# Kernel optimization log

Hardware: AMD Instinct MI355X
Metric: run time of the kernel (lower is better)

## Reference

```python
import jax, jax.numpy as jnp
import numpy as np

B, T, E, S, H = 1, 2048, 768, 256, 150
E3, E9 = 3 * E, 9 * E


def _lin(k, fan_in, fan_out):
    return jax.random.normal(k, (fan_in, fan_out), jnp.float32) / np.sqrt(fan_in).astype(np.float32)


def _mlp(x, W1, b1, W2, b2, W3, b3):
    # Score module: Linear -> ReLU -> Linear -> ReLU -> Linear (dropout = identity in eval)
    h = jax.nn.relu(x @ W1 + b1)
    h = jax.nn.relu(h @ W2 + b2)
    return h @ W3 + b3


def setup_inputs() -> dict:
    key = jax.random.key(0)
    ks = jax.random.split(key, 16)
    encoded_docs = jax.random.normal(ks[0], (B, T, E), jnp.float32)
    span_start = jnp.sort(jax.random.randint(ks[1], (B, S), 0, T - 16), axis=-1)
    span_width = jax.random.randint(ks[2], (B, S), 0, 16)
    return {
        'encoded_docs': encoded_docs,
        'span_start': span_start,
        'span_width': span_width,
        # attention Score (input dim E)
        'aW1': _lin(ks[3], E, H), 'ab1': jnp.zeros((H,), jnp.float32),
        'aW2': _lin(ks[4], H, H), 'ab2': jnp.zeros((H,), jnp.float32),
        'aW3': _lin(ks[5], H, 1), 'ab3': jnp.zeros((1,), jnp.float32),
        # mention Score (input dim 3E)
        'mW1': _lin(ks[6], E3, H), 'mb1': jnp.zeros((H,), jnp.float32),
        'mW2': _lin(ks[7], H, H), 'mb2': jnp.zeros((H,), jnp.float32),
        'mW3': _lin(ks[8], H, 1), 'mb3': jnp.zeros((1,), jnp.float32),
        # pairwise Score (input dim 9E)
        'pW1': _lin(ks[9], E9, H), 'pb1': jnp.zeros((H,), jnp.float32),
        'pW2': _lin(ks[10], H, H), 'pb2': jnp.zeros((H,), jnp.float32),
        'pW3': _lin(ks[11], H, 1), 'pb3': jnp.zeros((1,), jnp.float32),
    }


def reference(encoded_docs, span_start, span_width,
              aW1, ab1, aW2, ab2, aW3, ab3,
              mW1, mb1, mW2, mb2, mW3, mb3,
              pW1, pb1, pW2, pb2, pW3, pb3):
    e = encoded_docs  # [B, T, E]
    attn = _mlp(e, aW1, ab1, aW2, ab2, aW3, ab3)  # [B, T, 1]
    # span sums via prefix sums of attn-weighted embeddings (inclusive start..end)
    c = jnp.cumsum(e * attn, axis=1)  # [B, T, E]
    cpad = jnp.concatenate([jnp.zeros_like(c[:, :1]), c], axis=1)  # [B, T+1, E]
    end = jnp.clip(span_start + span_width, 0, T - 1)  # [B, S]
    bidx = jnp.arange(e.shape[0])[:, None]
    e_start = e[bidx, span_start]                      # [B, S, E]
    e_end = e[bidx, end]                               # [B, S, E]
    span_sum = cpad[bidx, end + 1] - cpad[bidx, span_start]  # [B, S, E]
    g = jnp.concatenate([e_start, e_end, span_sum], axis=-1)  # [B, S, 3E]
    m = _mlp(g, mW1, mb1, mW2, mb2, mW3, mb3)  # [B, S, 1]
    # pairwise: concat(g_i, g_j, g_i*g_j) @ pW1 decomposed over the three blocks
    Wa, Wb, Wc = pW1[:E3], pW1[E3:2 * E3], pW1[2 * E3:]
    hi = g @ Wa  # [B, S, H]
    hj = g @ Wb  # [B, S, H]
    hij = jnp.einsum('bie,bje,eh->bijh', g, g, Wc)  # [B, S, S, H]
    h1 = jax.nn.relu(hi[:, :, None, :] + hj[:, None, :, :] + hij + pb1)
    h2 = jax.nn.relu(h1 @ pW2 + pb2)
    s = h2 @ pW3 + pb3  # [B, S, S, 1]
    ext = (m[:, :, None, :] + m[:, None, :, :] + s) / 3.0
    return jnp.clip(ext, 0.0, 1.0)
```

## Files before the change

### kernel.cpp

```cpp
#include <hip/hip_runtime.h>

typedef unsigned short u16;
typedef unsigned int   u32;
typedef short bf16x8 __attribute__((ext_vector_type(8)));
typedef float f32x4  __attribute__((ext_vector_type(4)));

__device__ __forceinline__ u16 f2bf(float f) {
  union { float f; u32 u; } v; v.f = f;
  u32 u = v.u;
  u += 0x7fffu + ((u >> 16) & 1u);
  return (u16)(u >> 16);
}

__device__ __forceinline__ void splitbf(float x, u16& hi, u16& lo) {
  hi = f2bf(x);
  union { u32 u; float f; } r; r.u = (u32)hi << 16;
  lo = f2bf(x - r.f);
}

__device__ __forceinline__ float bflo(u32 p) {
  union { u32 u; float f; } v; v.u = p << 16; return v.f;
}
__device__ __forceinline__ float bfhi(u32 p) {
  union { u32 u; float f; } v; v.u = p & 0xffff0000u; return v.f;
}
__device__ __forceinline__ u32 cvtpk(float lo, float hi) {
  u32 r;
  asm("v_cvt_pk_bf16_f32 %0, %1, %2" : "=v"(r) : "v"(lo), "v"(hi));
  return r;
}
__device__ __forceinline__ void gload_lds16(const void* src, void* dst) {
  __builtin_amdgcn_global_load_lds(
      (const __attribute__((address_space(1))) u32*)src,
      (__attribute__((address_space(3))) u32*)dst, 16, 0, 0);
}

__global__ __launch_bounds__(256) void k_prepT(
    const float* __restrict__ mW1, const float* __restrict__ pW1,
    const float* __restrict__ aW1, const float* __restrict__ aW2,
    const float* __restrict__ mW2, const float* __restrict__ pW2,
    const float* __restrict__ pb1, const float* __restrict__ pb2,
    const float* __restrict__ pW3,
    u16* __restrict__ Wcath, u16* __restrict__ Wcatl,
    u16* __restrict__ aW1Th, u16* __restrict__ aW1Tl,
    u16* __restrict__ Wckg,
    float* __restrict__ aW2p, float* __restrict__ mW2p,
    u16* __restrict__ W2kg, float* __restrict__ pb1p,
    float* __restrict__ pb2p, float* __restrict__ w3p) {
  __shared__ float ls[64][153];
  const int tid = threadIdx.x;
  const int task = blockIdx.y;
  const int e0 = blockIdx.x * 64;
  if (task == 5) {
    const int stride = 36 * 256;
    const int t0 = blockIdx.x * 256 + tid;
    for (int t = t0; t < 152*160; t += stride) {
      int k = t / 160, h = t % 160;
      bool ok = (k < 150 && h < 150);
      aW2p[t] = ok ? aW2[k*150 + h] : 0.f;
      mW2p[t] = ok ? mW2[k*150 + h] : 0.f;
    }
    for (int t = t0; t < 24*1280; t += stride) {
      int kg = t / 1280, rem = t % 1280;
      int s = rem / 160, n = rem % 160;
      int k = kg*8 + s;
      float v = (k < 150 && n < 150) ? pW2[k*150 + n] : 0.f;
      W2kg[(size_t)kg*1280 + n*8 + s] = f2bf(v);
    }
    for (int t = t0; t < 160; t += stride) {
      pb1p[t] = (t < 150) ? pb1[t] : 0.f;
      pb2p[t] = (t < 150) ? pb2[t] : 0.f;
      w3p[t]  = (t < 150) ? pW3[t] : 0.f;
    }
    return;
  }
  if (task == 3 && e0 >= 768) return;
  const float* src;
  if (task == 0)      src = mW1;
  else if (task == 1) src = pW1;
  else if (task == 2) src = pW1 + (size_t)2304 * 150;
  else if (task == 3) src = aW1;
  else                src = pW1 + (size_t)4608 * 150;
  for (int t = tid; t < 9600; t += 256) {
    int r = t / 150, c = t - r * 150;
    ls[r][c] = src[(size_t)(e0 + r) * 150 + c];
  }
  __syncthreads();
  if (task < 3) {
    u16* dh = Wcath + (size_t)task * 160 * 2304;
    u16* dl = Wcatl + (size_t)task * 160 * 2304;
    for (int t = tid; t < 10240; t += 256) {
      int n = t >> 6, r = t & 63;
      float v = (n < 150) ? ls[r][n] : 0.f;
      u16 h, l; splitbf(v, h, l);
      dh[(size_t)n * 2304 + e0 + r] = h;
      dl[(size_t)n * 2304 + e0 + r] = l;
    }
  } else if (task == 3) {
    for (int t = tid; t < 10240; t += 256) {
      int n = t >> 6, r = t & 63;
      float v = (n < 150) ? ls[r][n] : 0.f;
      u16 h, l; splitbf(v, h, l);
      aW1Th[(size_t)n * 768 + e0 + r] = h;
      aW1Tl[(size_t)n * 768 + e0 + r] = l;
    }
  } else {
    for (int t = tid; t < 10240; t += 256) {
      int n = t >> 6, r = t & 63;
      int e = e0 + r;
      float v = (n < 150) ? ls[r][n] : 0.f;
      Wckg[((size_t)(e >> 3) * 160 + n) * 8 + (e & 7)] = f2bf(v);
    }
  }
}

__global__ __launch_bounds__(256) void k_attn1(
    const float* __restrict__ e, const u16* __restrict__ Wh,
    const u16* __restrict__ Wl, float* __restrict__ h1p) {
  __shared__ u16 lXh[32*64], lXl[32*64], lWh[160*64], lWl[160*64];
  const int tid = threadIdx.x, lane = tid & 63, w = tid >> 6;
  const int wm = w & 1, wh = w >> 1;
  const int m0 = blockIdx.x * 32;
  const int z  = blockIdx.y;
  f32x4 acc[5] = {};
  for (int e0 = z*192; e0 < (z+1)*192; e0 += 64) {
    {
      int r = tid >> 3, ec = tid & 7;
      const float* src = e + (size_t)(m0 + r)*768 + e0 + ec*8;
      float4 x0 = *(const float4*)src, x1 = *(const float4*)(src + 4);
      float xs[8] = {x0.x,x0.y,x0.z,x0.w,x1.x,x1.y,x1.z,x1.w};
      u16 hb[8], lb[8];
#pragma unroll
      for (int q = 0; q < 8; ++q) splitbf(xs[q], hb[q], lb[q]);
      int off = (r*128 + ec*16) ^ ((r & 7) << 4);
      *(uint4*)((char*)lXh + off) = make_uint4(
        (u32)hb[0]|((u32)hb[1]<<16), (u32)hb[2]|((u32)hb[3]<<16),
        (u32)hb[4]|((u32)hb[5]<<16), (u32)hb[6]|((u32)hb[7]<<16));
      *(uint4*)((char*)lXl + off) = make_uint4(
        (u32)lb[0]|((u32)lb[1]<<16), (u32)lb[2]|((u32)lb[3]<<16),
        (u32)lb[4]|((u32)lb[5]<<16), (u32)lb[6]|((u32)lb[7]<<16));
    }
#pragma unroll
    for (int t = 0; t < 5; ++t) {
      int c = tid + t*256;
      int h = c >> 3, ec = c & 7;
      int off = (h*128 + ec*16) ^ ((h & 7) << 4);
      *(uint4*)((char*)lWh + off) = *(const uint4*)(Wh + (size_t)h*768 + e0 + ec*8);
      *(uint4*)((char*)lWl + off) = *(const uint4*)(Wl + (size_t)h*768 + e0 + ec*8);
    }
    __syncthreads();
#pragma unroll
    for (int ks = 0; ks < 2; ++ks) {
      int eb = ks*64 + ((lane >> 4) << 4);
      int ar = wm*16 + (lane & 15);
      bf16x8 Ah = *(const bf16x8*)((const char*)lXh + ((ar*128 + eb) ^ ((ar & 7) << 4)));
      bf16x8 Al = *(const bf16x8*)((const char*)lXl + ((ar*128 + eb) ^ ((ar & 7) << 4)));
#pragma unroll
      for (int t = 0; t < 5; ++t) {
        int br = wh*80 + t*16 + (lane & 15);
        bf16x8 Bh = *(const bf16x8*)((const char*)lWh + ((br*128 + eb) ^ ((br & 7) << 4)));
        bf16x8 Bl = *(const bf16x8*)((const char*)lWl + ((br*128 + eb) ^ ((br & 7) << 4)));
        acc[t] = __builtin_amdgcn_mfma_f32_16x16x32_bf16(Ah, Bh, acc[t], 0, 0, 0);
        acc[t] = __builtin_amdgcn_mfma_f32_16x16x32_bf16(Al, Bh, acc[t], 0, 0, 0);
        acc[t] = __builtin_amdgcn_mfma_f32_16x16x32_bf16(Ah, Bl, acc[t], 0, 0, 0);
      }
    }
    __syncthreads();
  }
#pragma unroll
  for (int t = 0; t < 5; ++t) {
    int n = wh*80 + t*16 + (lane & 15);
#pragma unroll
    for (int r = 0; r < 4; ++r) {
      int m = m0 + wm*16 + ((lane >> 4) << 2) + r;
      h1p[((size_t)z*2048 + m)*160 + n] = acc[t][r];
    }
  }
}

__global__ __launch_bounds__(256) void k_attn2(
    const float* __restrict__ h1p, const float* __restrict__ W2p,
    const float* __restrict__ b1, const float* __restrict__ b2,
    const float* __restrict__ w3, const float* __restrict__ b3,
    float* __restrict__ attn) {
  __shared__ float hs[8][160];
  const int tid = threadIdx.x;
  const int t0 = blockIdx.x * 8;
  for (int idx = tid; idx < 1280; idx += 256) {
    int m = idx / 160, h = idx - m * 160;
    float s = 0.f;
#pragma unroll
    for (int z = 0; z < 4; ++z)
      s += h1p[((size_t)z*2048 + t0 + m)*160 + h];
    hs[m][h] = (h < 150) ? fmaxf(s + b1[h], 0.f) : 0.f;
  }
  __syncthreads();
  const int sp = tid >> 5, hb = tid & 31;
  float a2[5] = {0.f,0.f,0.f,0.f,0.f};
  for (int k = 0; k < 150; ++k) {
    float x = hs[sp][k];
#pragma unroll
    for (int q = 0; q < 5; ++q) a2[q] = fmaf(x, W2p[k*160 + hb + 32*q], a2[q]);
  }
  float p = 0.f;
#pragma unroll
  for (int q = 0; q < 5; ++q) {
    int h = hb + 32*q;
    if (h < 150) p += fmaxf(a2[q] + b2[h], 0.f) * w3[h];
  }
  p += __shfl_xor(p, 16, 32);
  p += __shfl_xor(p, 8, 32);
  p += __shfl_xor(p, 4, 32);
  p += __shfl_xor(p, 2, 32);
  p += __shfl_xor(p, 1, 32);
  if (hb == 0) attn[t0 + sp] = p + b3[0];
}

__global__ __launch_bounds__(256) void k_spans(
    const float* __restrict__ e, const float* __restrict__ attn,
    const int* __restrict__ sstart, const int* __restrict__ swidth,
    float* __restrict__ g, u16* __restrict__ gkg) {
  const int s = blockIdx.x;
  int st = sstart[s];
  int en = st + swidth[s];
  if (en > 2047) en = 2047;
  if (en < 0) en = 0;
  const int tid = threadIdx.x;
  for (int d = tid; d < 768; d += 256) {
    float v0 = e[(size_t)st*768 + d];
    float v1 = e[(size_t)en*768 + d];
    float acc = 0.f;
    for (int t = st; t <= en; ++t) acc += e[(size_t)t*768 + d] * attn[t];
    g[s*2304 + d]        = v0;
    g[s*2304 + 768 + d]  = v1;
    g[s*2304 + 1536 + d] = acc;
    int c0 = d, c1 = 768 + d, c2 = 1536 + d;
    gkg[((size_t)(c0>>3)*256 + s)*8 + (c0&7)] = f2bf(v0);
    gkg[((size_t)(c1>>3)*256 + s)*8 + (c1&7)] = f2bf(v1);
    gkg[((size_t)(c2>>3)*256 + s)*8 + (c2&7)] = f2bf(acc);
  }
}

__global__ __launch_bounds__(128) void k_span1(
    const float* __restrict__ g, const u16* __restrict__ Wh,
    const u16* __restrict__ Wl, float* __restrict__ pp) {
  __shared__ u16 lXh[16*64], lXl[16*64], lWh[160*64], lWl[160*64];
  const int tid = threadIdx.x, lane = tid & 63;
  const int wh = tid >> 6;
  const int m0 = blockIdx.x * 16;
  const int n0 = blockIdx.y * 160;
  const int z  = blockIdx.z;
  f32x4 acc[5] = {};
  for (int e0 = z*384; e0 < (z+1)*384; e0 += 64) {
    {
      int r = tid >> 3, ec = tid & 7;
      const float* src = g + (size_t)(m0 + r)*2304 + e0 + ec*8;
      float4 x0 = *(const float4*)src, x1 = *(const float4*)(src + 4);
      float xs[8] = {x0.x,x0.y,x0.z,x0.w,x1.x,x1.y,x1.z,x1.w};
      u16 hb[8], lb[8];
#pragma unroll
      for (int q = 0; q < 8; ++q) splitbf(xs[q], hb[q], lb[q]);
      int off = (r*128 + ec*16) ^ ((r & 7) << 4);
      *(uint4*)((char*)lXh + off) = make_uint4(
        (u32)hb[0]|((u32)hb[1]<<16), (u32)hb[2]|((u32)hb[3]<<16),
        (u32)hb[4]|((u32)hb[5]<<16), (u32)hb[6]|((u32)hb[7]<<16));
      *(uint4*)((char*)lXl + off) = make_uint4(
        (u32)lb[0]|((u32)lb[1]<<16), (u32)lb[2]|((u32)lb[3]<<16),
        (u32)lb[4]|((u32)lb[5]<<16), (u32)lb[6]|((u32)lb[7]<<16));
    }
#pragma unroll
    for (int t = 0; t < 10; ++t) {
      int c = tid + t*128;
      int h = c >> 3, ec = c & 7;
      int off = (h*128 + ec*16) ^ ((h & 7) << 4);
      *(uint4*)((char*)lWh + off) = *(const uint4*)(Wh + (size_t)(n0 + h)*2304 + e0 + ec*8);
      *(uint4*)((char*)lWl + off) = *(const uint4*)(Wl + (size_t)(n0 + h)*2304 + e0 + ec*8);
    }
    __syncthreads();
#pragma unroll
    for (int ks = 0; ks < 2; ++ks) {
      int eb = ks*64 + ((lane >> 4) << 4);
      int ar = lane & 15;
      bf16x8 Ah = *(const bf16x8*)((const char*)lXh + ((ar*128 + eb) ^ ((ar & 7) << 4)));
      bf16x8 Al = *(const bf16x8*)((const char*)lXl + ((ar*128 + eb) ^ ((ar & 7) << 4)));
#pragma unroll
      for (int t = 0; t < 5; ++t) {
        int br = wh*80 + t*16 + (lane & 15);
        bf16x8 Bh = *(const bf16x8*)((const char*)lWh + ((br*128 + eb) ^ ((br & 7) << 4)));
        bf16x8 Bl = *(const bf16x8*)((const char*)lWl + ((br*128 + eb) ^ ((br & 7) << 4)));
        acc[t] = __builtin_amdgcn_mfma_f32_16x16x32_bf16(Ah, Bh, acc[t], 0, 0, 0);
        acc[t] = __builtin_amdgcn_mfma_f32_16x16x32_bf16(Al, Bh, acc[t], 0, 0, 0);
        acc[t] = __builtin_amdgcn_mfma_f32_16x16x32_bf16(Ah, Bl, acc[t], 0, 0, 0);
      }
    }
    __syncthreads();
  }
#pragma unroll
  for (int t = 0; t < 5; ++t) {
    int nc = n0 + wh*80 + t*16 + (lane & 15);
#pragma unroll
    for (int r = 0; r < 4; ++r) {
      int m = m0 + ((lane >> 4) << 2) + r;
      pp[((size_t)z*256 + m)*480 + nc] = acc[t][r];
    }
  }
}

__global__ __launch_bounds__(256) void k_span2r(
    const float* __restrict__ pp, const float* __restrict__ mb1,
    const float* __restrict__ W2p, const float* __restrict__ b2,
    const float* __restrict__ w3, const float* __restrict__ b3,
    float* __restrict__ hi, float* __restrict__ hj, float* __restrict__ mo) {
  __shared__ float hs[8][160];
  const int tid = threadIdx.x;
  const int s0 = blockIdx.x * 8;
  for (int idx = tid; idx < 3840; idx += 256) {
    int mr = idx / 480, n = idx - mr * 480;
    int m = s0 + mr;
    float s = 0.f;
#pragma unroll
    for (int z = 0; z < 6; ++z) s += pp[((size_t)z*256 + m)*480 + n];
    if (n < 160)      hs[mr][n] = (n < 150) ? fmaxf(s + mb1[n], 0.f) : 0.f;
    else if (n < 320) hi[m*160 + n - 160] = s;
    else              hj[m*160 + n - 320] = s;
  }
  __syncthreads();
  const int sp = tid >> 5, hb = tid & 31;
  float a2[5] = {0.f,0.f,0.f,0.f,0.f};
  for (int k = 0; k < 150; ++k) {
    float x = hs[sp][k];
#pragma unroll
    for (int q = 0; q < 5; ++q) a2[q] = fmaf(x, W2p[k*160 + hb + 32*q], a2[q]);
  }
  float p = 0.f;
#pragma unroll
  for (int q = 0; q < 5; ++q) {
    int h = hb + 32*q;
    if (h < 150) p += fmaxf(a2[q] + b2[h], 0.f) * w3[h];
  }
  p += __shfl_xor(p, 16, 32);
  p += __shfl_xor(p, 8, 32);
  p += __shfl_xor(p, 4, 32);
  p += __shfl_xor(p, 2, 32);
  p += __shfl_xor(p, 1, 32);
  if (hb == 0) mo[s0 + sp] = p + b3[0];
}

__global__ __launch_bounds__(512, 2) void k_hij7(
    const float* __restrict__ g, const u16* __restrict__ gkg,
    const u16* __restrict__ Wckg, const float* __restrict__ hi,
    const float* __restrict__ hj, const float* __restrict__ pb1p,
    const u16* __restrict__ W2kg, const float* __restrict__ pb2p,
    const float* __restrict__ w3p, const float* __restrict__ pb3,
    const float* __restrict__ mv, float* __restrict__ out) {
  __shared__ __align__(16) char smem[104448];
  const int tid = threadIdx.x, lane = tid & 63, w = tid >> 6;
  const int wj = w & 3, wh = w >> 2;
  const int i = blockIdx.x;
  const float* grow = g + (size_t)i * 2304;

  f32x4 acc[4][5] = {};
  bf16x8 afC[8];
  uint4 wcR[3];
  float4 gA[3], gB[3];

  const u16* pA = gkg + (((lane >> 4) * 256) + wj * 64 + (lane & 15)) * 8;
  const int ep0 = (tid / 160) * 8;
  const int ep1 = ((tid + 512) / 160) * 8;
  const int ep2 = ((tid + 1024) / 160) * 8;
  const int bB = (((lane >> 4) * 160) + wh * 80 + (lane & 15)) * 16;

  auto loadA = [&](int t) {
    const u16* p = pA + (size_t)t * 16384;
#pragma unroll
    for (int ks = 0; ks < 2; ++ks)
#pragma unroll
      for (int q = 0; q < 4; ++q)
        afC[ks * 4 + q] = *(const bf16x8*)(p + ks * 8192 + q * 128);
  };
  auto loadB = [&](int t) {
    const u16* wp = Wckg + (size_t)t * 10240;
    const float* gp = grow + t * 64;
    wcR[0] = *(const uint4*)(wp + (size_t)tid * 8);
    gA[0] = *(const float4*)(gp + ep0); gB[0] = *(const float4*)(gp + ep0 + 4);
    wcR[1] = *(const uint4*)(wp + (size_t)(tid + 512) * 8);
    gA[1] = *(const float4*)(gp + ep1); gB[1] = *(const float4*)(gp + ep1 + 4);
    if (tid < 256) {
      wcR[2] = *(const uint4*)(wp + (size_t)(tid + 1024) * 8);
      gA[2] = *(const float4*)(gp + ep2); gB[2] = *(const float4*)(gp + ep2 + 4);
    }
  };
  auto writeB = [&](int buf) {
    char* base = smem + buf * 20480;
#pragma unroll
    for (int z = 0; z < 2; ++z) {
      uint4 v = wcR[z]; float4 ga = gA[z], gb = gB[z];
      uint4 r;
      r.x = cvtpk(bflo(v.x) * ga.x, bfhi(v.x) * ga.y);
      r.y = cvtpk(bflo(v.y) * ga.z, bfhi(v.y) * ga.w);
      r.z = cvtpk(bflo(v.z) * gb.x, bfhi(v.z) * gb.y);
      r.w = cvtpk(bflo(v.w) * gb.z, bfhi(v.w) * gb.w);
      *(uint4*)(base + (tid + z * 512) * 16) = r;
    }
    if (tid < 256) {
      uint4 v = wcR[2]; float4 ga = gA[2], gb = gB[2];
      uint4 r;
      r.x = cvtpk(bflo(v.x) * ga.x, bfhi(v.x) * ga.y);
      r.y = cvtpk(bflo(v.y) * ga.z, bfhi(v.y) * ga.w);
      r.z = cvtpk(bflo(v.z) * gb.x, bfhi(v.z) * gb.y);
      r.w = cvtpk(bflo(v.w) * gb.z, bfhi(v.w) * gb.w);
      *(uint4*)(base + (tid + 1024) * 16) = r;
    }
  };

  loadB(0);
  loadA(0);
  writeB(0);
  asm volatile("s_waitcnt lgkmcnt(0)" ::: "memory");
  __builtin_amdgcn_s_barrier();
  __builtin_amdgcn_sched_barrier(0);

  for (int t = 0; t < 36; ++t) {
    const int buf = t & 1;
    if (t < 35) loadB(t + 1);
    const char* Bb = smem + buf * 20480;
    __builtin_amdgcn_s_setprio(1);
#pragma unroll
    for (int ks = 0; ks < 2; ++ks) {
#pragma unroll
      for (int u = 0; u < 5; ++u) {
        bf16x8 bfr = *(const bf16x8*)(Bb + bB + ks * 10240 + u * 256);
#pragma unroll
        for (int q = 0; q < 4; ++q)
          acc[q][u] = __builtin_amdgcn_mfma_f32_16x16x32_bf16(
              afC[ks * 4 + q], bfr, acc[q][u], 0, 0, 0);
      }
    }
    __builtin_amdgcn_s_setprio(0);
    if (t < 35) { loadA(t + 1); writeB(buf ^ 1); }
    asm volatile("s_waitcnt lgkmcnt(0)" ::: "memory");
    __builtin_amdgcn_s_barrier();
    __builtin_amdgcn_sched_barrier(0);
  }

  {
    float hib[5];
#pragma unroll
    for (int u = 0; u < 5; ++u) {
      int h = wh * 80 + u * 16 + (lane & 15);
      hib[u] = hi[i * 160 + h] + pb1p[h];
    }
#pragma unroll
    for (int q = 0; q < 4; ++q) {
      int jl = wj * 64 + q * 16 + ((lane >> 4) << 2);
#pragma unroll
      for (int r = 0; r < 4; ++r) {
        const float* hjr = hj + (size_t)(jl + r) * 160;
#pragma unroll
        for (int u = 0; u < 5; ++u) {
          int h = wh * 80 + u * 16 + (lane & 15);
          float v = fmaxf(acc[q][u][r] + hib[u] + hjr[h], 0.f);
          *(u16*)(smem + ((h >> 3) * 256 + jl + r) * 16 + (h & 7) * 2) = f2bf(v);
        }
      }
    }
  }
  __syncthreads();

  f32x4 acc2[4][5] = {};
  for (int c = 0; c < 3; ++c) {
    const int G64 = (c < 2) ? 20 : 10;
    for (int g0 = w; g0 < G64; g0 += 8) {
      const u16* src = W2kg + ((size_t)c * 1280 + g0 * 64 + lane) * 8;
      gload_lds16(src, smem + 81920 + g0 * 1024);
    }
    __syncthreads();
    const int nks = (c < 2) ? 2 : 1;
    for (int ks = 0; ks < nks; ++ks) {
      const int kl = ks * 4 + (lane >> 4);
      bf16x8 af2[4];
#pragma unroll
      for (int q = 0; q < 4; ++q)
        af2[q] = *(const bf16x8*)(smem + ((c * 8 + kl) * 256 + wj * 64 + q * 16 + (lane & 15)) * 16);
#pragma unroll
      for (int u = 0; u < 5; ++u) {
        bf16x8 b2 = *(const bf16x8*)(smem + 81920 + (kl * 160 + wh * 80 + u * 16 + (lane & 15)) * 16);
#pragma unroll
        for (int q = 0; q < 4; ++q)
          acc2[q][u] = __builtin_amdgcn_mfma_f32_16x16x32_bf16(af2[q], b2, acc2[q][u], 0, 0, 0);
      }
    }
    __syncthreads();
  }

  {
    float w3v[5], b2v[5];
#pragma unroll
    for (int u = 0; u < 5; ++u) {
      int h2 = wh * 80 + u * 16 + (lane & 15);
      w3v[u] = w3p[h2]; b2v[u] = pb2p[h2];
    }
#pragma unroll
    for (int q = 0; q < 4; ++q) {
#pragma unroll
      for (int r = 0; r < 4; ++r) {
        float sp = 0.f;
#pragma unroll
        for (int u = 0; u < 5; ++u)
          sp += fmaxf(acc2[q][u][r] + b2v[u], 0.f) * w3v[u];
        sp += __shfl_xor(sp, 1);
        sp += __shfl_xor(sp, 2);
        sp += __shfl_xor(sp, 4);
        sp += __shfl_xor(sp, 8);
        if ((lane & 15) == 0) {
          int jl = wj * 64 + q * 16 + ((lane >> 4) << 2) + r;
          *(float*)(smem + 102400 + (jl * 2 + wh) * 4) = sp;
        }
      }
    }
  }
  __syncthreads();
  if (tid < 256) {
    float s = *(const float*)(smem + 102400 + tid * 8) +
              *(const float*)(smem + 102400 + tid * 8 + 4) + pb3[0];
    float v = (mv[i] + mv[tid] + s) * (1.f / 3.f);
    out[i * 256 + tid] = fminf(fmaxf(v, 0.f), 1.f);
  }
}

extern "C" void kernel_launch(void* const* d_in, const int* in_sizes, int n_in,
                              void* d_out, int out_size, void* d_ws, size_t ws_size,
                              hipStream_t stream) {
  (void)in_sizes; (void)n_in; (void)out_size; (void)ws_size;
  const float* e    = (const float*)d_in[0];
  const int*   sst  = (const int*)d_in[1];
  const int*   swd  = (const int*)d_in[2];
  const float* aW1  = (const float*)d_in[3];
  const float* ab1  = (const float*)d_in[4];
  const float* aW2  = (const float*)d_in[5];
  const float* ab2  = (const float*)d_in[6];
  const float* aW3  = (const float*)d_in[7];
  const float* ab3  = (const float*)d_in[8];
  const float* mW1  = (const float*)d_in[9];
  const float* mb1  = (const float*)d_in[10];
  const float* mW2  = (const float*)d_in[11];
  const float* mb2  = (const float*)d_in[12];
  const float* mW3  = (const float*)d_in[13];
  const float* mb3  = (const float*)d_in[14];
  const float* pW1  = (const float*)d_in[15];
  const float* pb1  = (const float*)d_in[16];
  const float* pW2  = (const float*)d_in[17];
  const float* pb2  = (const float*)d_in[18];
  const float* pW3  = (const float*)d_in[19];
  const float* pb3  = (const float*)d_in[20];
  float* out = (float*)d_out;

  char* ws = (char*)d_ws;
  size_t off = 0;
  auto alloc = [&](size_t bytes) -> char* {
    char* p = ws + off;
    off += (bytes + 255) & ~(size_t)255;
    return p;
  };
  float* attn  = (float*)alloc(2048ULL*4);
  float* g     = (float*)alloc(256ULL*2304*4);
  float* hi    = (float*)alloc(256ULL*160*4);
  float* hj    = (float*)alloc(256ULL*160*4);
  float* mv    = (float*)alloc(256ULL*4);
  float* h1p   = (float*)alloc(4ULL*2048*160*4);
  float* pp    = (float*)alloc(6ULL*256*480*4);
  u16*   aW1Th = (u16*)alloc(160ULL*768*2);
  u16*   aW1Tl = (u16*)alloc(160ULL*768*2);
  u16*   Wcath = (u16*)alloc(480ULL*2304*2);
  u16*   Wcatl = (u16*)alloc(480ULL*2304*2);
  float* aW2p  = (float*)alloc(152ULL*160*4);
  float* mW2p  = (float*)alloc(152ULL*160*4);
  u16*   gkg   = (u16*)alloc(288ULL*256*8*2);
  u16*   Wckg  = (u16*)alloc(288ULL*160*8*2);
  u16*   W2kg  = (u16*)alloc(24ULL*1280*2);
  float* pb1p  = (float*)alloc(160ULL*4);
  float* pb2p  = (float*)alloc(160ULL*4);
  float* w3p   = (float*)alloc(160ULL*4);

  k_prepT<<<dim3(36, 6), 256, 0, stream>>>(mW1, pW1, aW1, aW2, mW2, pW2,
                                           pb1, pb2, pW3,
                                           Wcath, Wcatl, aW1Th, aW1Tl, Wckg,
                                           aW2p, mW2p, W2kg, pb1p, pb2p, w3p);
  k_attn1<<<dim3(64, 4), 256, 0, stream>>>(e, aW1Th, aW1Tl, h1p);
  k_attn2<<<256, 256, 0, stream>>>(h1p, aW2p, ab1, ab2, aW3, ab3, attn);
  k_spans<<<256, 256, 0, stream>>>(e, attn, sst, swd, g, gkg);
  k_span1<<<dim3(16, 3, 6), 128, 0, stream>>>(g, Wcath, Wcatl, pp);
  k_span2r<<<32, 256, 0, stream>>>(pp, mb1, mW2p, mb2, mW3, mb3, hi, hj, mv);
  k_hij7<<<256, 512, 0, stream>>>(g, gkg, Wckg, hi, hj, pb1p,
                                  W2kg, pb2p, w3p, pb3, mv, out);
}
```

Before: 134.2 us.

## Stream Wc tiles directly to LDS and apply g_i scaling to A fragments

The pairwise hij kernel no longer loads Wc into registers, multiplies by the row's g_i and writes to LDS. Wc tiles now go straight from global memory to LDS through direct async loads, and the g_i scaling moves onto the A-operand fragments (gkg) in registers just before the MFMAs. A fragments and g values are double-buffered in registers with vmcnt-based waits, so more loads overlap compute. This removes the VALU conversion and LDS write traffic per tile, but adds per-iteration conversion on the A side and more register pressure. It depends on the gload_lds16 helper and on the vmcnt counts being correct.

```diff
diff --git a/kernel.cpp b/kernel.cpp
--- a/kernel.cpp
+++ b/kernel.cpp
@@ -346,7 +346,7 @@
   if (hb == 0) mo[s0 + sp] = p + b3[0];
 }
 
-__global__ __launch_bounds__(512, 2) void k_hij7(
+__global__ __launch_bounds__(512, 2) void k_hij9(
     const float* __restrict__ g, const u16* __restrict__ gkg,
     const u16* __restrict__ Wckg, const float* __restrict__ hi,
     const float* __restrict__ hj, const float* __restrict__ pb1p,
@@ -360,85 +360,83 @@
   const float* grow = g + (size_t)i * 2304;
 
   f32x4 acc[4][5] = {};
-  bf16x8 afC[8];
-  uint4 wcR[3];
-  float4 gA[3], gB[3];
+  bf16x8 afC[8], afN[8];
+  float4 gsC[4], gsN[4];
 
   const u16* pA = gkg + (((lane >> 4) * 256) + wj * 64 + (lane & 15)) * 8;
-  const int ep0 = (tid / 160) * 8;
-  const int ep1 = ((tid + 512) / 160) * 8;
-  const int ep2 = ((tid + 1024) / 160) * 8;
+  const float* pG = grow + (lane >> 4) * 8;
   const int bB = (((lane >> 4) * 160) + wh * 80 + (lane & 15)) * 16;
 
-  auto loadA = [&](int t) {
+  auto issueB = [&](int buf, int t) {
+    const u16* src = Wckg + (size_t)t * 10240 + lane * 8;
+    char* dst = smem + buf * 20480;
+    gload_lds16(src + (w * 2 + 0) * 512, dst + (w * 2 + 0) * 1024);
+    gload_lds16(src + (w * 2 + 1) * 512, dst + (w * 2 + 1) * 1024);
+    if (w < 4) gload_lds16(src + (16 + w) * 512, dst + (16 + w) * 1024);
+  };
+  auto loadA = [&](int t, bf16x8* af, float4* gs) {
     const u16* p = pA + (size_t)t * 16384;
 #pragma unroll
-    for (int ks = 0; ks < 2; ++ks)
+    for (int ks = 0; ks < 2; ++ks) {
 #pragma unroll
       for (int q = 0; q < 4; ++q)
-        afC[ks * 4 + q] = *(const bf16x8*)(p + ks * 8192 + q * 128);
+        af[ks * 4 + q] = *(const bf16x8*)(p + ks * 8192 + q * 128);
+      const float* gp = pG + t * 64 + ks * 32;
+      gs[ks * 2 + 0] = *(const float4*)gp;
+      gs[ks * 2 + 1] = *(const float4*)(gp + 4);
+    }
   };
-  auto loadB = [&](int t) {
-    const u16* wp = Wckg + (size_t)t * 10240;
-    const float* gp = grow + t * 64;
-    wcR[0] = *(const uint4*)(wp + (size_t)tid * 8);
-    gA[0] = *(const float4*)(gp + ep0); gB[0] = *(const float4*)(gp + ep0 + 4);
-    wcR[1] = *(const uint4*)(wp + (size_t)(tid + 512) * 8);
-    gA[1] = *(const float4*)(gp + ep1); gB[1] = *(const float4*)(gp + ep1 + 4);
-    if (tid < 256) {
-      wcR[2] = *(const uint4*)(wp + (size_t)(tid + 1024) * 8);
-      gA[2] = *(const float4*)(gp + ep2); gB[2] = *(const float4*)(gp + ep2 + 4);
-    }
-  };
-  auto writeB = [&](int buf) {
-    char* base = smem + buf * 20480;
-#pragma unroll
-    for (int z = 0; z < 2; ++z) {
-      uint4 v = wcR[z]; float4 ga = gA[z], gb = gB[z];
-      uint4 r;
-      r.x = cvtpk(bflo(v.x) * ga.x, bfhi(v.x) * ga.y);
-      r.y = cvtpk(bflo(v.y) * ga.z, bfhi(v.y) * ga.w);
-      r.z = cvtpk(bflo(v.z) * gb.x, bfhi(v.z) * gb.y);
-      r.w = cvtpk(bflo(v.w) * gb.z, bfhi(v.w) * gb.w);
-      *(uint4*)(base + (tid + z * 512) * 16) = r;
-    }
-    if (tid < 256) {
-      uint4 v = wcR[2]; float4 ga = gA[2], gb = gB[2];
-      uint4 r;
-      r.x = cvtpk(bflo(v.x) * ga.x, bfhi(v.x) * ga.y);
-      r.y = cvtpk(bflo(v.y) * ga.z, bfhi(v.y) * ga.w);
-      r.z = cvtpk(bflo(v.z) * gb.x, bfhi(v.z) * gb.y);
-      r.w = cvtpk(bflo(v.w) * gb.z, bfhi(v.w) * gb.w);
-      *(uint4*)(base + (tid + 1024) * 16) = r;
-    }
-  };
-
-  loadB(0);
-  loadA(0);
-  writeB(0);
-  asm volatile("s_waitcnt lgkmcnt(0)" ::: "memory");
+
+  issueB(0, 0);
+  __builtin_amdgcn_sched_barrier(0);
+  loadA(0, afC, gsC);
+  __builtin_amdgcn_sched_barrier(0);
+  asm volatile("s_waitcnt vmcnt(12)" ::: "memory");
   __builtin_amdgcn_s_barrier();
   __builtin_amdgcn_sched_barrier(0);
 
   for (int t = 0; t < 36; ++t) {
     const int buf = t & 1;
-    if (t < 35) loadB(t + 1);
+    if (t < 35) {
+      issueB(buf ^ 1, t + 1);
+      __builtin_amdgcn_sched_barrier(0);
+      loadA(t + 1, afN, gsN);
+    }
+    __builtin_amdgcn_sched_barrier(0);
     const char* Bb = smem + buf * 20480;
     __builtin_amdgcn_s_setprio(1);
 #pragma unroll
     for (int ks = 0; ks < 2; ++ks) {
+      const float4 ga = gsC[ks * 2], gb = gsC[ks * 2 + 1];
+      bf16x8 as[4];
+#pragma unroll
+      for (int q = 0; q < 4; ++q) {
+        union { bf16x8 b; uint4 u; } v, r;
+        v.b = afC[ks * 4 + q];
+        r.u.x = cvtpk(bflo(v.u.x) * ga.x, bfhi(v.u.x) * ga.y);
+        r.u.y = cvtpk(bflo(v.u.y) * ga.z, bfhi(v.u.y) * ga.w);
+        r.u.z = cvtpk(bflo(v.u.z) * gb.x, bfhi(v.u.z) * gb.y);
+        r.u.w = cvtpk(bflo(v.u.w) * gb.z, bfhi(v.u.w) * gb.w);
+        as[q] = r.b;
+      }
 #pragma unroll
       for (int u = 0; u < 5; ++u) {
         bf16x8 bfr = *(const bf16x8*)(Bb + bB + ks * 10240 + u * 256);
 #pragma unroll
         for (int q = 0; q < 4; ++q)
           acc[q][u] = __builtin_amdgcn_mfma_f32_16x16x32_bf16(
-              afC[ks * 4 + q], bfr, acc[q][u], 0, 0, 0);
+              as[q], bfr, acc[q][u], 0, 0, 0);
       }
     }
     __builtin_amdgcn_s_setprio(0);
-    if (t < 35) { loadA(t + 1); writeB(buf ^ 1); }
-    asm volatile("s_waitcnt lgkmcnt(0)" ::: "memory");
+    if (t < 35) {
+#pragma unroll
+      for (int k = 0; k < 8; ++k) afC[k] = afN[k];
+#pragma unroll
+      for (int k = 0; k < 4; ++k) gsC[k] = gsN[k];
+    }
+    __builtin_amdgcn_sched_barrier(0);
+    asm volatile("s_waitcnt vmcnt(12) lgkmcnt(0)" ::: "memory");
     __builtin_amdgcn_s_barrier();
     __builtin_amdgcn_sched_barrier(0);
   }
@@ -591,6 +589,6 @@
   k_spans<<<256, 256, 0, stream>>>(e, attn, sst, swd, g, gkg);
   k_span1<<<dim3(16, 3, 6), 128, 0, stream>>>(g, Wcath, Wcatl, pp);
   k_span2r<<<32, 256, 0, stream>>>(pp, mb1, mW2p, mb2, mW3, mb3, hi, hj, mv);
-  k_hij7<<<256, 512, 0, stream>>>(g, gkg, Wckg, hi, hj, pb1p,
+  k_hij9<<<256, 512, 0, stream>>>(g, gkg, Wckg, hi, hj, pb1p,
                                   W2kg, pb2p, w3p, pb3, mv, out);
 }
```

New measurement: 162.8 us (median of 3 runs). 21.3% more time.
